# Performance work log

Measured on AMD Instinct MI355X. Metric: run time of the kernel, lower is better.

The kernel has to match this reference:

```python
import jax, jax.numpy as jnp
import numpy as np

N, F_IN, HEADS, D_HEAD, HID, OUT, E = 50000, 128, 4, 64, 256, 2, 800000
NEG_SLOPE = 0.2


def setup_inputs() -> dict:
    key = jax.random.key(0)
    ks = jax.random.split(key, 12)
    x = jax.random.normal(ks[0], (N, F_IN), dtype=jnp.float32)
    edge_index = jax.random.randint(ks[1], (2, E), 0, N, dtype=jnp.int64)
    s = 0.05
    W_gat = jax.random.normal(ks[2], (F_IN, HEADS * D_HEAD), dtype=jnp.float32) * s
    att_src = jax.random.normal(ks[3], (HEADS, D_HEAD), dtype=jnp.float32) * s
    att_dst = jax.random.normal(ks[4], (HEADS, D_HEAD), dtype=jnp.float32) * s
    b_gat = jnp.zeros((HEADS * D_HEAD,), dtype=jnp.float32)
    W1 = jax.random.normal(ks[5], (HEADS * D_HEAD, HID), dtype=jnp.float32) * s
    b1 = jnp.zeros((HID,), dtype=jnp.float32)
    W2 = jax.random.normal(ks[6], (HID, HID), dtype=jnp.float32) * s
    b2 = jnp.zeros((HID,), dtype=jnp.float32)
    W3 = jax.random.normal(ks[7], (HID, OUT), dtype=jnp.float32) * s
    b3 = jnp.zeros((OUT,), dtype=jnp.float32)
    return {"x": x, "edge_index": edge_index, "W_gat": W_gat, "att_src": att_src,
            "att_dst": att_dst, "b_gat": b_gat, "W1": W1, "b1": b1,
            "W2": W2, "b2": b2, "W3": W3, "b3": b3}


def _gat(x, edge_index, W_gat, att_src, att_dst, b_gat):
    n = x.shape[0]
    loop = jnp.arange(n, dtype=edge_index.dtype)
    src = jnp.concatenate([edge_index[0], loop])  # [E+N] message sources j
    dst = jnp.concatenate([edge_index[1], loop])  # [E+N] message targets i
    h = (x @ W_gat).reshape(n, HEADS, D_HEAD)      # [N,H,D]
    a_s = jnp.einsum('nhd,hd->nh', h, att_src)     # [N,H]
    a_d = jnp.einsum('nhd,hd->nh', h, att_dst)     # [N,H]
    e = a_s[src] + a_d[dst]                        # [E',H]
    e = jax.nn.leaky_relu(e, NEG_SLOPE)
    # per-destination-node softmax over incoming edges (numerically stable)
    emax = jax.ops.segment_max(e, dst, num_segments=n)
    e = jnp.exp(e - emax[dst])
    denom = jax.ops.segment_sum(e, dst, num_segments=n)
    alpha = e / denom[dst]                         # [E',H]
    msg = h[src] * alpha[:, :, None]               # [E',H,D]
    out = jax.ops.segment_sum(msg, dst, num_segments=n)  # [N,H,D]
    return out.reshape(n, HEADS * D_HEAD) + b_gat


def reference(x, edge_index, W_gat, att_src, att_dst, b_gat, W1, b1, W2, b2, W3, b3):
    h = _gat(x, edge_index, W_gat, att_src, att_dst, b_gat)
    h = jax.nn.relu(h @ W1 + b1)
    h = jax.nn.relu(h @ W2 + b2)
    return h @ W3 + b3
```

## Files before the change

kernel.cpp:

```cpp
#include <hip/hip_runtime.h>
#include <math.h>

#define N_NODES 50000
#define NP 50048
#define F_IN 128
#define HD 256
#define HID 256
#define NE 800000
#define CAP 64
#define NEG_SLOPE 0.2f
#define G1_BLOCKS (NP / 64)
#define FILL_BLOCKS ((NE + 1023) / 1024)
#define CNT_STRIDE 4

typedef __attribute__((ext_vector_type(8))) __bf16 bf16x8;
typedef __attribute__((ext_vector_type(4))) __bf16 bf16x4;
typedef __attribute__((ext_vector_type(4))) float f32x4;

#define GLD_LDS16(g, l)                                                      \
    __builtin_amdgcn_global_load_lds(                                        \
        (const __attribute__((address_space(1))) unsigned int*)(g),          \
        (__attribute__((address_space(3))) unsigned int*)(l), 16, 0, 0)

#define PB_INIT 196
#define PB_WG   128
#define PB_W1   256
#define PB_W2   256

__global__ __launch_bounds__(256) void prep_kernel(const float* __restrict__ Wg,
                                                   const float* __restrict__ W1,
                                                   const float* __restrict__ W2,
                                                   __bf16* __restrict__ Wg_t,
                                                   __bf16* __restrict__ W1_t,
                                                   __bf16* __restrict__ W2_t,
                                                   int* __restrict__ cnt,
                                                   unsigned short* __restrict__ bucket) {
    int b = blockIdx.x, t = threadIdx.x;
    if (b < PB_INIT) {
        int n = b * 256 + t;
        if (n < N_NODES) { cnt[(size_t)n * CNT_STRIDE] = 1; bucket[n * CAP] = (unsigned short)n; }
    } else if (b < PB_INIT + PB_WG) {
        int i = (b - PB_INIT) * 256 + t;
        int m = i >> 7, k = i & 127;
        Wg_t[i] = (__bf16)Wg[(size_t)k * HD + m];
    } else if (b < PB_INIT + PB_WG + PB_W1) {
        int i = (b - PB_INIT - PB_WG) * 256 + t;
        int m = i >> 8, k = i & 255;
        W1_t[i] = (__bf16)W1[(size_t)k * HID + m];
    } else {
        int i = (b - PB_INIT - PB_WG - PB_W1) * 256 + t;
        int m = i >> 8, k = i & 255;
        W2_t[i] = (__bf16)W2[(size_t)k * HID + m];
    }
}

__global__ __launch_bounds__(256) void g1_fill_kernel(const float* __restrict__ x,
                                                      const __bf16* __restrict__ Bt,
                                                      const float* __restrict__ att_src,
                                                      const float* __restrict__ att_dst,
                                                      const int* __restrict__ ew,
                                                      __bf16* __restrict__ h,
                                                      float* __restrict__ a_s,
                                                      float* __restrict__ a_d,
                                                      int* __restrict__ cnt,
                                                      unsigned short* __restrict__ bucket) {
    __shared__ __bf16 As[64 * 32];
    __shared__ __bf16 Bs[256 * 32];

    if (blockIdx.x >= G1_BLOCKS) {
        const int base = (blockIdx.x - G1_BLOCKS) * 1024 + threadIdx.x;
        const int e0 = base, e1 = base + 256, e2 = base + 512, e3 = base + 768;
        const bool v0 = e0 < NE, v1 = e1 < NE, v2 = e2 < NE, v3 = e3 < NE;
        long long p0 = 0, p1 = 0, p2 = 0, p3 = 0;
        if (v0) p0 = *(const long long*)&ew[2 * e0];
        if (v1) p1 = *(const long long*)&ew[2 * e1];
        if (v2) p2 = *(const long long*)&ew[2 * e2];
        if (v3) p3 = *(const long long*)&ew[2 * e3];
        const int hiall = (int)(p0 >> 32) | (int)(p1 >> 32) |
                          (int)(p2 >> 32) | (int)(p3 >> 32);
        unsigned long long bal = __ballot(hiall != 0);
        int s0 = 0, s1 = 0, s2 = 0, s3 = 0, d0 = 0, d1 = 0, d2 = 0, d3 = 0;
        if (bal == 0) {
            s0 = (int)p0; s1 = (int)p1; s2 = (int)p2; s3 = (int)p3;
            if (v0) d0 = ew[2 * NE + 2 * e0];
            if (v1) d1 = ew[2 * NE + 2 * e1];
            if (v2) d2 = ew[2 * NE + 2 * e2];
            if (v3) d3 = ew[2 * NE + 2 * e3];
        } else {
            if (v0) { s0 = ew[e0]; d0 = ew[NE + e0]; }
            if (v1) { s1 = ew[e1]; d1 = ew[NE + e1]; }
            if (v2) { s2 = ew[e2]; d2 = ew[NE + e2]; }
            if (v3) { s3 = ew[e3]; d3 = ew[NE + e3]; }
        }
        int pos0 = CAP, pos1 = CAP, pos2 = CAP, pos3 = CAP;
        if (v0) pos0 = atomicAdd(&cnt[(size_t)d0 * CNT_STRIDE], 1);
        if (v1) pos1 = atomicAdd(&cnt[(size_t)d1 * CNT_STRIDE], 1);
        if (v2) pos2 = atomicAdd(&cnt[(size_t)d2 * CNT_STRIDE], 1);
        if (v3) pos3 = atomicAdd(&cnt[(size_t)d3 * CNT_STRIDE], 1);
        if (pos0 < CAP) bucket[d0 * CAP + pos0] = (unsigned short)s0;
        if (pos1 < CAP) bucket[d1 * CAP + pos1] = (unsigned short)s1;
        if (pos2 < CAP) bucket[d2 * CAP + pos2] = (unsigned short)s2;
        if (pos3 < CAP) bucket[d3 * CAP + pos3] = (unsigned short)s3;
        return;
    }

    const int t = threadIdx.x;
    const int lane = t & 63, wv = t >> 6;
    const int lr = lane & 15, q = lane >> 4, lk = q * 8;
    const int col_off = wv * 64;
    const int row0 = blockIdx.x * 64;
    const int sr = t >> 2, sk = (t & 3) * 8;
    const int arow = row0 + sr;
    const bool avalid = arow < N_NODES;

    f32x4 acc[4][4];
#pragma unroll
    for (int r = 0; r < 4; ++r)
#pragma unroll
        for (int c = 0; c < 4; ++c) acc[r][c] = f32x4{0.f, 0.f, 0.f, 0.f};

    for (int k0 = 0; k0 < F_IN; k0 += 32) {
        float4 v0 = {0, 0, 0, 0}, v1 = {0, 0, 0, 0};
        if (avalid) {
            const float* xp = &x[(size_t)arow * F_IN + k0 + sk];
            v0 = *(const float4*)xp;
            v1 = *(const float4*)(xp + 4);
        }
        bf16x8 o;
        o[0] = (__bf16)v0.x; o[1] = (__bf16)v0.y; o[2] = (__bf16)v0.z; o[3] = (__bf16)v0.w;
        o[4] = (__bf16)v1.x; o[5] = (__bf16)v1.y; o[6] = (__bf16)v1.z; o[7] = (__bf16)v1.w;
        *(bf16x8*)&As[sr * 32 + sk] = o;
#pragma unroll
        for (int s = 0; s < 4; ++s) {
            int r = s * 64 + sr;
            GLD_LDS16(&Bt[(size_t)r * F_IN + k0 + sk], &Bs[r * 32 + sk]);
        }
        __syncthreads();
        bf16x8 af[4], bfr[4];
#pragma unroll
        for (int i = 0; i < 4; ++i) {
            af[i]  = *(const bf16x8*)&As[(i * 16 + lr) * 32 + lk];
            bfr[i] = *(const bf16x8*)&Bs[(col_off + i * 16 + lr) * 32 + lk];
        }
#pragma unroll
        for (int r = 0; r < 4; ++r)
#pragma unroll
            for (int c = 0; c < 4; ++c)
                acc[r][c] = __builtin_amdgcn_mfma_f32_16x16x32_bf16(af[r], bfr[c], acc[r][c], 0, 0, 0);
        __syncthreads();
    }

    float asv[4], adv[4];
#pragma unroll
    for (int c = 0; c < 4; ++c) {
        int col = col_off + c * 16 + lr;
        asv[c] = att_src[col];
        adv[c] = att_dst[col];
    }
    float ps[4][4], pd[4][4];
#pragma unroll
    for (int r = 0; r < 4; ++r)
#pragma unroll
        for (int i = 0; i < 4; ++i) { ps[r][i] = 0.f; pd[r][i] = 0.f; }

#pragma unroll
    for (int c = 0; c < 4; ++c) {
        int col = col_off + c * 16 + lr;
#pragma unroll
        for (int r = 0; r < 4; ++r) {
#pragma unroll
            for (int i = 0; i < 4; ++i) {
                int row = row0 + r * 16 + q * 4 + i;
                float v = acc[r][c][i];
                h[(size_t)row * HD + col] = (__bf16)v;
                ps[r][i] += v * asv[c];
                pd[r][i] += v * adv[c];
            }
        }
    }
#pragma unroll
    for (int r = 0; r < 4; ++r)
#pragma unroll
        for (int i = 0; i < 4; ++i) {
#pragma unroll
            for (int m = 1; m < 16; m <<= 1) {
                ps[r][i] += __shfl_xor(ps[r][i], m);
                pd[r][i] += __shfl_xor(pd[r][i], m);
            }
        }
    if (lr == 0) {
#pragma unroll
        for (int r = 0; r < 4; ++r)
#pragma unroll
            for (int i = 0; i < 4; ++i) {
                int row = row0 + r * 16 + q * 4 + i;
                a_s[row * 4 + wv] = ps[r][i];
                a_d[row * 4 + wv] = pd[r][i];
            }
    }
}

__device__ __forceinline__ float lrelu(float v) { return v >= 0.f ? v : NEG_SLOPE * v; }

__global__ __launch_bounds__(64) void gat_aggregate_kernel(const __bf16* __restrict__ h,
                                                           const float* __restrict__ a_s,
                                                           const float* __restrict__ a_d,
                                                           const int* __restrict__ cnt,
                                                           const unsigned short* __restrict__ bucket,
                                                           const float* __restrict__ b_gat,
                                                           __bf16* __restrict__ gat) {
    __shared__ unsigned short s_src[128];
    __shared__ float s_alpha[128];
    const int lane = threadIdx.x;
    const int g = blockIdx.x & 7;
    const int pair = blockIdx.x >> 3;
    const int half = lane >> 5;
    const int l32 = lane & 31;
    const int n = pair * 2 + half;
    const int head = g >> 1;
    const int c0 = g * 32;

    int deg = cnt[(size_t)n * CNT_STRIDE];
    if (deg > CAP) deg = CAP;
    const float ad = a_d[n * 4 + head];

    int src0 = n, src1 = n;
    float e0 = -1e30f, e1 = -1e30f;
    if (l32 < deg) {
        src0 = bucket[n * CAP + l32];
        e0 = lrelu(a_s[src0 * 4 + head] + ad);
    }
    if (l32 + 32 < deg) {
        src1 = bucket[n * CAP + l32 + 32];
        e1 = lrelu(a_s[src1 * 4 + head] + ad);
    }
    float m = fmaxf(e0, e1);
#pragma unroll
    for (int off = 1; off < 32; off <<= 1) m = fmaxf(m, __shfl_xor(m, off));
    float w0 = (l32 < deg) ? __expf(e0 - m) : 0.f;
    float w1 = (l32 + 32 < deg) ? __expf(e1 - m) : 0.f;
    float s = w0 + w1;
#pragma unroll
    for (int off = 1; off < 32; off <<= 1) s += __shfl_xor(s, off);
    const float inv = 1.f / s;
    s_src[half * 64 + l32] = (unsigned short)src0;
    s_src[half * 64 + l32 + 32] = (unsigned short)src1;
    s_alpha[half * 64 + l32] = w0 * inv;
    s_alpha[half * 64 + l32 + 32] = w1 * inv;
    __syncthreads();

    const int slot = l32 >> 3;
    const int cq = l32 & 7;
    float acc0 = 0.f, acc1 = 0.f, acc2 = 0.f, acc3 = 0.f;
    for (int j = slot; j < deg; j += 4) {
        int sj = s_src[half * 64 + j];
        float aj = s_alpha[half * 64 + j];
        bf16x4 hv = *(const bf16x4*)&h[(size_t)sj * HD + c0 + cq * 4];
        acc0 += aj * (float)hv[0];
        acc1 += aj * (float)hv[1];
        acc2 += aj * (float)hv[2];
        acc3 += aj * (float)hv[3];
    }
#pragma unroll
    for (int off = 8; off <= 16; off <<= 1) {
        acc0 += __shfl_xor(acc0, off);
        acc1 += __shfl_xor(acc1, off);
        acc2 += __shfl_xor(acc2, off);
        acc3 += __shfl_xor(acc3, off);
    }
    if (slot == 0) {
        const float* bg = &b_gat[c0 + cq * 4];
        bf16x4 o;
        o[0] = (__bf16)(acc0 + bg[0]);
        o[1] = (__bf16)(acc1 + bg[1]);
        o[2] = (__bf16)(acc2 + bg[2]);
        o[3] = (__bf16)(acc3 + bg[3]);
        *(bf16x4*)&gat[(size_t)n * HD + c0 + cq * 4] = o;
    }
}

__global__ __launch_bounds__(256) void fused_mlp_kernel(const __bf16* __restrict__ A,
                                                        const __bf16* __restrict__ W1t,
                                                        const __bf16* __restrict__ W2t,
                                                        const float* __restrict__ b1,
                                                        const float* __restrict__ b2,
                                                        const float* __restrict__ W3,
                                                        const float* __restrict__ b3,
                                                        float* __restrict__ out) {
    __shared__ __bf16 As[64 * 32];
    __shared__ __bf16 Ws[256 * 32];
    __shared__ __bf16 h1s[8 * 64 * 32];
    __shared__ float s_out[64][2];
    const int t = threadIdx.x;
    const int lane = t & 63, wv = t >> 6;
    const int lr = lane & 15, q = lane >> 4, lk = q * 8;
    const int col_off = wv * 64;
    const int row0 = blockIdx.x * 64;
    const int sr = t >> 2, sk = (t & 3) * 8;

    if (t < 128) ((float*)s_out)[t] = 0.f;

    f32x4 acc[4][4];
#pragma unroll
    for (int r = 0; r < 4; ++r)
#pragma unroll
        for (int c = 0; c < 4; ++c) acc[r][c] = f32x4{0.f, 0.f, 0.f, 0.f};

    for (int k0 = 0; k0 < HD; k0 += 32) {
        GLD_LDS16(&A[(size_t)(row0 + sr) * HD + k0 + sk], &As[sr * 32 + sk]);
#pragma unroll
        for (int s = 0; s < 4; ++s) {
            int r = s * 64 + sr;
            GLD_LDS16(&W1t[(size_t)r * HD + k0 + sk], &Ws[r * 32 + sk]);
        }
        __syncthreads();
        bf16x8 af[4], bfr[4];
#pragma unroll
        for (int i = 0; i < 4; ++i) {
            af[i]  = *(const bf16x8*)&As[(i * 16 + lr) * 32 + lk];
            bfr[i] = *(const bf16x8*)&Ws[(col_off + i * 16 + lr) * 32 + lk];
        }
#pragma unroll
        for (int r = 0; r < 4; ++r)
#pragma unroll
            for (int c = 0; c < 4; ++c)
                acc[r][c] = __builtin_amdgcn_mfma_f32_16x16x32_bf16(af[r], bfr[c], acc[r][c], 0, 0, 0);
        __syncthreads();
    }
#pragma unroll
    for (int c = 0; c < 4; ++c) {
        int col = col_off + c * 16 + lr;
        float bv = b1[col];
        int cb = (col >> 5) * 2048;
        int kk = col & 31;
#pragma unroll
        for (int r = 0; r < 4; ++r)
#pragma unroll
            for (int i = 0; i < 4; ++i) {
                int row = r * 16 + q * 4 + i;
                float v = fmaxf(acc[r][c][i] + bv, 0.f);
                h1s[cb + row * 32 + kk] = (__bf16)v;
                acc[r][c][i] = 0.f;
            }
    }
    __syncthreads();

    for (int k0 = 0; k0 < HID; k0 += 32) {
#pragma unroll
        for (int s = 0; s < 4; ++s) {
            int r = s * 64 + sr;
            GLD_LDS16(&W2t[(size_t)r * HID + k0 + sk], &Ws[r * 32 + sk]);
        }
        __syncthreads();
        const int cb = (k0 >> 5) * 2048;
        bf16x8 af[4], bfr[4];
#pragma unroll
        for (int i = 0; i < 4; ++i) {
            af[i]  = *(const bf16x8*)&h1s[cb + (i * 16 + lr) * 32 + lk];
            bfr[i] = *(const bf16x8*)&Ws[(col_off + i * 16 + lr) * 32 + lk];
        }
#pragma unroll
        for (int r = 0; r < 4; ++r)
#pragma unroll
            for (int c = 0; c < 4; ++c)
                acc[r][c] = __builtin_amdgcn_mfma_f32_16x16x32_bf16(af[r], bfr[c], acc[r][c], 0, 0, 0);
        __syncthreads();
    }

    float b2v[4], w30[4], w31[4];
#pragma unroll
    for (int c = 0; c < 4; ++c) {
        int col = col_off + c * 16 + lr;
        b2v[c] = b2[col];
        w30[c] = W3[col * 2];
        w31[c] = W3[col * 2 + 1];
    }
#pragma unroll
    for (int r = 0; r < 4; ++r) {
#pragma unroll
        for (int i = 0; i < 4; ++i) {
            float o0 = 0.f, o1 = 0.f;
#pragma unroll
            for (int c = 0; c < 4; ++c) {
                float v = fmaxf(acc[r][c][i] + b2v[c], 0.f);
                o0 += v * w30[c];
                o1 += v * w31[c];
            }
#pragma unroll
            for (int m = 1; m < 16; m <<= 1) {
                o0 += __shfl_xor(o0, m);
                o1 += __shfl_xor(o1, m);
            }
            if (lr == 0) {
                int row = r * 16 + q * 4 + i;
                atomicAdd(&s_out[row][0], o0);
                atomicAdd(&s_out[row][1], o1);
            }
        }
    }
    __syncthreads();
    if (t < 128) {
        int row = t >> 1, o = t & 1;
        int g = row0 + row;
        if (g < N_NODES) out[g * 2 + o] = s_out[row][o] + b3[o];
    }
}

extern "C" void kernel_launch(void* const* d_in, const int* in_sizes, int n_in,
                              void* d_out, int out_size, void* d_ws, size_t ws_size,
                              hipStream_t stream) {
    const float* x       = (const float*)d_in[0];
    const int*   ei      = (const int*)d_in[1];
    const float* W_gat   = (const float*)d_in[2];
    const float* att_src = (const float*)d_in[3];
    const float* att_dst = (const float*)d_in[4];
    const float* b_gat   = (const float*)d_in[5];
    const float* W1      = (const float*)d_in[6];
    const float* b1      = (const float*)d_in[7];
    const float* W2      = (const float*)d_in[8];
    const float* b2      = (const float*)d_in[9];
    const float* W3      = (const float*)d_in[10];
    const float* b3      = (const float*)d_in[11];
    float* out = (float*)d_out;

    char* ws = (char*)d_ws;
    __bf16* h_bf   = (__bf16*)ws;  ws += (size_t)NP * HD * 2;
    __bf16* gat_bf = (__bf16*)ws;  ws += (size_t)NP * HD * 2;
    __bf16* Wg_t   = (__bf16*)ws;  ws += (size_t)HD * F_IN * 2;
    __bf16* W1_t   = (__bf16*)ws;  ws += (size_t)HID * HD * 2;
    __bf16* W2_t   = (__bf16*)ws;  ws += (size_t)HID * HID * 2;
    float* a_s     = (float*)ws;   ws += (size_t)NP * 4 * 4;
    float* a_d     = (float*)ws;   ws += (size_t)NP * 4 * 4;
    int* cnt       = (int*)ws;     ws += (size_t)N_NODES * CNT_STRIDE * 4;
    unsigned short* bucket = (unsigned short*)ws;
    ws += (size_t)N_NODES * CAP * 2;

    prep_kernel<<<PB_INIT + PB_WG + PB_W1 + PB_W2, 256, 0, stream>>>(
        W_gat, W1, W2, Wg_t, W1_t, W2_t, cnt, bucket);
    g1_fill_kernel<<<G1_BLOCKS + FILL_BLOCKS, 256, 0, stream>>>(
        x, Wg_t, att_src, att_dst, ei, h_bf, a_s, a_d, cnt, bucket);
    gat_aggregate_kernel<<<(N_NODES / 2) * 8, 64, 0, stream>>>(h_bf, a_s, a_d, cnt,
                                                               bucket, b_gat, gat_bf);
    fused_mlp_kernel<<<NP / 64, 256, 0, stream>>>(gat_bf, W1_t, W2_t, b1, b2, W3, b3, out);
}
```

Before: 294.3 us.

## Make GAT aggregation persistent with XCD-affine column groups and atomic work queue

Replaces the one-block-per-(node pair, column group) aggregation launch with a persistent kernel of 2048 256-thread blocks. Each block reads its XCD id from a hardware register, starts on the column group matching that XCD, and pulls chunks of node pairs from a per-group atomic cursor that is reset in the prep kernel. The intent is to keep each 32-column slice of h resident in one XCD's L2 and to cut launch and scheduling overhead. Gathers are also widened to 8 bf16 per lane. In exchange it adds atomic traffic, more block-level barriers per chunk, and relies on an undocumented hardware-register encoding for the XCD id.

```diff
diff --git a/kernel.cpp b/kernel.cpp
--- a/kernel.cpp
+++ b/kernel.cpp
@@ -13,6 +13,10 @@
 #define FILL_BLOCKS ((NE + 1023) / 1024)
 #define CNT_STRIDE 4
 
+#define PAIRS (N_NODES / 2)
+#define CHUNK_PAIRS 32
+#define GAT_BLOCKS 2048
+
 typedef __attribute__((ext_vector_type(8))) __bf16 bf16x8;
 typedef __attribute__((ext_vector_type(4))) __bf16 bf16x4;
 typedef __attribute__((ext_vector_type(4))) float f32x4;
@@ -34,9 +38,11 @@
                                                    __bf16* __restrict__ W1_t,
                                                    __bf16* __restrict__ W2_t,
                                                    int* __restrict__ cnt,
-                                                   unsigned short* __restrict__ bucket) {
+                                                   unsigned short* __restrict__ bucket,
+                                                   int* __restrict__ cursors) {
     int b = blockIdx.x, t = threadIdx.x;
     if (b < PB_INIT) {
+        if (b == 0 && t < 8) cursors[t] = 0;
         int n = b * 256 + t;
         if (n < N_NODES) { cnt[(size_t)n * CNT_STRIDE] = 1; bucket[n * CAP] = (unsigned short)n; }
     } else if (b < PB_INIT + PB_WG) {
@@ -202,80 +208,100 @@
 
 __device__ __forceinline__ float lrelu(float v) { return v >= 0.f ? v : NEG_SLOPE * v; }
 
-__global__ __launch_bounds__(64) void gat_aggregate_kernel(const __bf16* __restrict__ h,
-                                                           const float* __restrict__ a_s,
-                                                           const float* __restrict__ a_d,
-                                                           const int* __restrict__ cnt,
-                                                           const unsigned short* __restrict__ bucket,
-                                                           const float* __restrict__ b_gat,
-                                                           __bf16* __restrict__ gat) {
-    __shared__ unsigned short s_src[128];
-    __shared__ float s_alpha[128];
-    const int lane = threadIdx.x;
-    const int g = blockIdx.x & 7;
-    const int pair = blockIdx.x >> 3;
-    const int half = lane >> 5;
-    const int l32 = lane & 31;
-    const int n = pair * 2 + half;
-    const int head = g >> 1;
-    const int c0 = g * 32;
-
-    int deg = cnt[(size_t)n * CNT_STRIDE];
-    if (deg > CAP) deg = CAP;
-    const float ad = a_d[n * 4 + head];
-
-    int src0 = n, src1 = n;
-    float e0 = -1e30f, e1 = -1e30f;
-    if (l32 < deg) {
-        src0 = bucket[n * CAP + l32];
-        e0 = lrelu(a_s[src0 * 4 + head] + ad);
-    }
-    if (l32 + 32 < deg) {
-        src1 = bucket[n * CAP + l32 + 32];
-        e1 = lrelu(a_s[src1 * 4 + head] + ad);
-    }
-    float m = fmaxf(e0, e1);
-#pragma unroll
-    for (int off = 1; off < 32; off <<= 1) m = fmaxf(m, __shfl_xor(m, off));
-    float w0 = (l32 < deg) ? __expf(e0 - m) : 0.f;
-    float w1 = (l32 + 32 < deg) ? __expf(e1 - m) : 0.f;
-    float s = w0 + w1;
-#pragma unroll
-    for (int off = 1; off < 32; off <<= 1) s += __shfl_xor(s, off);
-    const float inv = 1.f / s;
-    s_src[half * 64 + l32] = (unsigned short)src0;
-    s_src[half * 64 + l32 + 32] = (unsigned short)src1;
-    s_alpha[half * 64 + l32] = w0 * inv;
-    s_alpha[half * 64 + l32 + 32] = w1 * inv;
-    __syncthreads();
-
-    const int slot = l32 >> 3;
-    const int cq = l32 & 7;
-    float acc0 = 0.f, acc1 = 0.f, acc2 = 0.f, acc3 = 0.f;
-    for (int j = slot; j < deg; j += 4) {
-        int sj = s_src[half * 64 + j];
-        float aj = s_alpha[half * 64 + j];
-        bf16x4 hv = *(const bf16x4*)&h[(size_t)sj * HD + c0 + cq * 4];
-        acc0 += aj * (float)hv[0];
-        acc1 += aj * (float)hv[1];
-        acc2 += aj * (float)hv[2];
-        acc3 += aj * (float)hv[3];
-    }
-#pragma unroll
-    for (int off = 8; off <= 16; off <<= 1) {
-        acc0 += __shfl_xor(acc0, off);
-        acc1 += __shfl_xor(acc1, off);
-        acc2 += __shfl_xor(acc2, off);
-        acc3 += __shfl_xor(acc3, off);
-    }
-    if (slot == 0) {
-        const float* bg = &b_gat[c0 + cq * 4];
-        bf16x4 o;
-        o[0] = (__bf16)(acc0 + bg[0]);
-        o[1] = (__bf16)(acc1 + bg[1]);
-        o[2] = (__bf16)(acc2 + bg[2]);
-        o[3] = (__bf16)(acc3 + bg[3]);
-        *(bf16x4*)&gat[(size_t)n * HD + c0 + cq * 4] = o;
+__global__ __launch_bounds__(256) void gat_aggregate_kernel(const __bf16* __restrict__ h,
+                                                            const float* __restrict__ a_s,
+                                                            const float* __restrict__ a_d,
+                                                            const int* __restrict__ cnt,
+                                                            const unsigned short* __restrict__ bucket,
+                                                            const float* __restrict__ b_gat,
+                                                            __bf16* __restrict__ gat,
+                                                            int* __restrict__ cursors) {
+    __shared__ unsigned short s_src[4][128];
+    __shared__ float s_alpha[4][128];
+    __shared__ int s_chunk;
+
+    const int t = threadIdx.x;
+    const int wv = t >> 6, lane = t & 63;
+    const int half = lane >> 5, l32 = lane & 31;
+    const int slot = l32 >> 2;
+    const int cq = l32 & 3;
+
+    const int my_xcd = (int)(__builtin_amdgcn_s_getreg(63508) & 7u);
+
+    for (int gi = 0; gi < 8; ++gi) {
+        const int g = (my_xcd + gi) & 7;
+        const int head = g >> 1;
+        const int c0 = g * 32;
+        for (;;) {
+            __syncthreads();
+            if (t == 0) s_chunk = atomicAdd(&cursors[g], CHUNK_PAIRS);
+            __syncthreads();
+            const int p0 = s_chunk;
+            if (p0 >= PAIRS) break;
+
+            for (int pp = wv; pp < CHUNK_PAIRS; pp += 4) {
+                const int pair = p0 + pp;
+                if (pair >= PAIRS) break;
+                const int n = pair * 2 + half;
+
+                int deg = cnt[(size_t)n * CNT_STRIDE];
+                if (deg > CAP) deg = CAP;
+                const float ad = a_d[n * 4 + head];
+
+                int src0 = n, src1 = n;
+                float e0 = -1e30f, e1 = -1e30f;
+                if (l32 < deg) {
+                    src0 = bucket[n * CAP + l32];
+                    e0 = lrelu(a_s[src0 * 4 + head] + ad);
+                }
+                if (l32 + 32 < deg) {
+                    src1 = bucket[n * CAP + l32 + 32];
+                    e1 = lrelu(a_s[src1 * 4 + head] + ad);
+                }
+                float m = fmaxf(e0, e1);
+#pragma unroll
+                for (int off = 1; off < 32; off <<= 1) m = fmaxf(m, __shfl_xor(m, off));
+                float w0 = (l32 < deg) ? __expf(e0 - m) : 0.f;
+                float w1 = (l32 + 32 < deg) ? __expf(e1 - m) : 0.f;
+                float s = w0 + w1;
+#pragma unroll
+                for (int off = 1; off < 32; off <<= 1) s += __shfl_xor(s, off);
+                const float inv = 1.f / s;
+                s_src[wv][half * 64 + l32] = (unsigned short)src0;
+                s_src[wv][half * 64 + l32 + 32] = (unsigned short)src1;
+                s_alpha[wv][half * 64 + l32] = w0 * inv;
+                s_alpha[wv][half * 64 + l32 + 32] = w1 * inv;
+                asm volatile("s_waitcnt lgkmcnt(0)" ::: "memory");
+
+                float acc[8];
+#pragma unroll
+                for (int k = 0; k < 8; ++k) acc[k] = 0.f;
+                const int hb = c0 + cq * 8;
+                for (int j = slot; j < deg; j += 8) {
+                    const int sj = s_src[wv][half * 64 + j];
+                    const float aj = s_alpha[wv][half * 64 + j];
+                    const bf16x8 hv = *(const bf16x8*)&h[(size_t)sj * HD + hb];
+#pragma unroll
+                    for (int k = 0; k < 8; ++k) acc[k] += aj * (float)hv[k];
+                }
+#pragma unroll
+                for (int k = 0; k < 8; ++k) {
+                    acc[k] += __shfl_xor(acc[k], 4);
+                    acc[k] += __shfl_xor(acc[k], 8);
+                    acc[k] += __shfl_xor(acc[k], 16);
+                }
+                if (slot == 0) {
+                    const float4 bg0 = *(const float4*)&b_gat[hb];
+                    const float4 bg1 = *(const float4*)&b_gat[hb + 4];
+                    bf16x8 o;
+                    o[0] = (__bf16)(acc[0] + bg0.x); o[1] = (__bf16)(acc[1] + bg0.y);
+                    o[2] = (__bf16)(acc[2] + bg0.z); o[3] = (__bf16)(acc[3] + bg0.w);
+                    o[4] = (__bf16)(acc[4] + bg1.x); o[5] = (__bf16)(acc[5] + bg1.y);
+                    o[6] = (__bf16)(acc[6] + bg1.z); o[7] = (__bf16)(acc[7] + bg1.w);
+                    *(bf16x8*)&gat[(size_t)n * HD + hb] = o;
+                }
+            }
+        }
     }
 }
 
@@ -432,14 +458,15 @@
     float* a_s     = (float*)ws;   ws += (size_t)NP * 4 * 4;
     float* a_d     = (float*)ws;   ws += (size_t)NP * 4 * 4;
     int* cnt       = (int*)ws;     ws += (size_t)N_NODES * CNT_STRIDE * 4;
+    int* cursors   = (int*)ws;     ws += 64;
     unsigned short* bucket = (unsigned short*)ws;
     ws += (size_t)N_NODES * CAP * 2;
 
     prep_kernel<<<PB_INIT + PB_WG + PB_W1 + PB_W2, 256, 0, stream>>>(
-        W_gat, W1, W2, Wg_t, W1_t, W2_t, cnt, bucket);
+        W_gat, W1, W2, Wg_t, W1_t, W2_t, cnt, bucket, cursors);
     g1_fill_kernel<<<G1_BLOCKS + FILL_BLOCKS, 256, 0, stream>>>(
         x, Wg_t, att_src, att_dst, ei, h_bf, a_s, a_d, cnt, bucket);
-    gat_aggregate_kernel<<<(N_NODES / 2) * 8, 64, 0, stream>>>(h_bf, a_s, a_d, cnt,
-                                                               bucket, b_gat, gat_bf);
+    gat_aggregate_kernel<<<GAT_BLOCKS, 256, 0, stream>>>(h_bf, a_s, a_d, cnt, bucket,
+                                                         b_gat, gat_bf, cursors);
     fused_mlp_kernel<<<NP / 64, 256, 0, stream>>>(gat_bf, W1_t, W2_t, b1, b2, W3, b3, out);
 }
```

New measurement: 490.0 us. 1.66x slower.
